# Performance work log

Measured on AMD Instinct MI355X. Metric: run time of the kernel, lower is better.

Reference implementation:

```python
import jax, jax.numpy as jnp
import numpy as np

B, N1, N2 = 2, 1024, 1024
D_MODEL, N_HEADS = 2048, 16
HEAD_DIM = D_MODEL // N_HEADS
EPS = 1e-6
ROPE_THETA = 10000.0


def _split_heads(qkv):
    # [b, n, 3*h*d] -> (q, k, v) each [b, h, n, d]
    b, n, _ = qkv.shape
    qkv = qkv.reshape(b, n, 3, N_HEADS, HEAD_DIM)
    qkv = jnp.transpose(qkv, (2, 0, 3, 1, 4))
    return qkv[0], qkv[1], qkv[2]


def _rmsnorm(x, gamma):
    # RMS norm over head dim with learned scale (QKNorm)
    inv = jax.lax.rsqrt(jnp.mean(jnp.square(x), axis=-1, keepdims=True) + EPS)
    return x * inv * gamma


def _rope(x, offset=0):
    # x: [b, h, n, d]; half-split rotary embedding
    n, d = x.shape[-2], x.shape[-1]
    inv_freq = 1.0 / (ROPE_THETA ** (jnp.arange(0, d, 2, dtype=jnp.float32) / d))
    pos = jnp.arange(n, dtype=jnp.float32) + offset
    ang = pos[:, None] * inv_freq  # [n, d/2]
    cos, sin = jnp.cos(ang), jnp.sin(ang)
    x1, x2 = jnp.split(x, 2, axis=-1)
    return jnp.concatenate([x1 * cos - x2 * sin, x1 * sin + x2 * cos], axis=-1)


def _attention(q, k, v):
    # dense path of flex_attention (block_mask=None): softmax(qk^T/sqrt(d)) v
    scale = 1.0 / np.sqrt(HEAD_DIM)
    scores = jnp.einsum('bhqd,bhkd->bhqk', q, k) * scale
    probs = jax.nn.softmax(scores, axis=-1)
    return jnp.einsum('bhqk,bhkd->bhqd', probs, v)


def setup_inputs() -> dict:
    key = jax.random.key(0)
    ks = jax.random.split(key, 8)
    w_std = 0.02
    return {
        'x_1': jax.random.normal(ks[0], (B, N1, D_MODEL), jnp.float32),
        'x_2': jax.random.normal(ks[1], (B, N2, D_MODEL), jnp.float32),
        'w_qkv1': jax.random.normal(ks[2], (D_MODEL, 3 * D_MODEL), jnp.float32) * w_std,
        'b_qkv1': jnp.zeros((3 * D_MODEL,), jnp.float32),
        'w_qkv2': jax.random.normal(ks[3], (D_MODEL, 3 * D_MODEL), jnp.float32) * w_std,
        'b_qkv2': jnp.zeros((3 * D_MODEL,), jnp.float32),
        'qg1': jnp.ones((HEAD_DIM,), jnp.float32),
        'kg1': jnp.ones((HEAD_DIM,), jnp.float32),
        'qg2': jnp.ones((HEAD_DIM,), jnp.float32),
        'kg2': jnp.ones((HEAD_DIM,), jnp.float32),
        'w_out1': jax.random.normal(ks[4], (D_MODEL, D_MODEL), jnp.float32) * w_std,
        'b_out1': jnp.zeros((D_MODEL,), jnp.float32),
        'w_out2': jax.random.normal(ks[5], (D_MODEL, D_MODEL), jnp.float32) * w_std,
        'b_out2': jnp.zeros((D_MODEL,), jnp.float32),
    }


def reference(x_1, x_2, w_qkv1, b_qkv1, w_qkv2, b_qkv2,
              qg1, kg1, qg2, kg2, w_out1, b_out1, w_out2, b_out2):
    n1 = x_1.shape[1]
    qs, ks_, vs = [], [], []
    for x, w, b, qg, kg in ((x_1, w_qkv1, b_qkv1, qg1, kg1),
                            (x_2, w_qkv2, b_qkv2, qg2, kg2)):
        q, k, v = _split_heads(x @ w + b)
        q, k = _rmsnorm(q, qg), _rmsnorm(k, kg)
        qs.append(q); ks_.append(k); vs.append(v)
    q = jnp.concatenate(qs, axis=-2)  # [b, h, n1+n2, d]
    k = jnp.concatenate(ks_, axis=-2)
    v = jnp.concatenate(vs, axis=-2)
    q, k = _rope(q), _rope(k)
    attn = _attention(q, k, v)
    # merge: b h n d -> b n (h d)
    b, h, n, d = attn.shape
    attn = jnp.transpose(attn, (0, 2, 1, 3)).reshape(b, n, h * d)
    out1 = attn[:, :n1] @ w_out1 + b_out1
    out2 = attn[:, n1:] @ w_out2 + b_out2
    return out1, out2
```

## Files before the change

kernel.cpp:

```cpp
#include <hip/hip_runtime.h>

#define DM   2048
#define NH   16
#define HD   128
#define QKVN 6144
#define NTOT 2048

typedef __bf16 bf16x8 __attribute__((ext_vector_type(8)));
typedef float  f32x4  __attribute__((ext_vector_type(4)));
typedef unsigned short ushort_t;

__device__ __forceinline__ unsigned short f2bf(float f) {
  union { float f; unsigned u; } v; v.f = f;
  return (unsigned short)((v.u + 0x7FFFu + ((v.u >> 16) & 1u)) >> 16);
}
__device__ __forceinline__ float bf2f(unsigned short u) {
  union { unsigned u; float f; } v; v.u = ((unsigned)u) << 16;
  return v.f;
}
__device__ __forceinline__ void glds16(const void* g, void* l) {
  __builtin_amdgcn_global_load_lds(
      (const __attribute__((address_space(1))) unsigned int*)g,
      (__attribute__((address_space(3))) unsigned int*)l, 16, 0, 0);
}
#define COMPILER_MEM_BARRIER() asm volatile("" ::: "memory")


__global__ __launch_bounds__(256) void prep_kernel(
    const float* __restrict__ wq1, const float* __restrict__ wq2,
    const float* __restrict__ wo1, const float* __restrict__ wo2,
    const float* __restrict__ x1,  const float* __restrict__ x2,
    ushort_t* __restrict__ wq1t, ushort_t* __restrict__ wq2t,
    ushort_t* __restrict__ wo1t, ushort_t* __restrict__ wo2t,
    ushort_t* __restrict__ xb1,  ushort_t* __restrict__ xb2,
    float2* __restrict__ rtab)
{
  __shared__ __align__(16) unsigned short Ls[64][72];
  const int bid = blockIdx.x, tid = threadIdx.x;
  if (bid < 8192) {
    const float* src; ushort_t* dst; int N, nb, kb;
    if (bid < 6144) {
      src = (bid < 3072) ? wq1 : wq2; dst = (bid < 3072) ? wq1t : wq2t;
      int id = bid % 3072; N = QKVN; nb = id % 96; kb = id / 96;
    } else {
      int id = bid - 6144;
      src = (id < 1024) ? wo1 : wo2; dst = (id < 1024) ? wo1t : wo2t;
      id %= 1024; N = DM; nb = id % 32; kb = id / 32;
    }
    int n0 = nb * 64, k0 = kb * 64;
#pragma unroll
    for (int it = 0; it < 4; ++it) {
      int row = (tid >> 4) + it * 16, c4 = (tid & 15) * 4;
      float4 v = *reinterpret_cast<const float4*>(&src[(size_t)(k0 + row) * N + n0 + c4]);
      Ls[c4 + 0][row] = f2bf(v.x); Ls[c4 + 1][row] = f2bf(v.y);
      Ls[c4 + 2][row] = f2bf(v.z); Ls[c4 + 3][row] = f2bf(v.w);
    }
    __syncthreads();
#pragma unroll
    for (int it = 0; it < 2; ++it) {
      int lin = tid + it * 256, r = lin >> 3, c8 = (lin & 7) * 8;
      *reinterpret_cast<uint4*>(&dst[(size_t)(n0 + r) * 2048 + k0 + c8]) =
          *reinterpret_cast<const uint4*>(&Ls[r][c8]);
    }
  } else if (bid < 10240) {
    int id = bid - 8192;
    const float* src = (id < 1024) ? x1 : x2;
    ushort_t* dst = (id < 1024) ? xb1 : xb2;
    id %= 1024;
    size_t base = (size_t)id * 4096;
#pragma unroll
    for (int it = 0; it < 4; ++it) {
      size_t i = base + (size_t)(it * 256 + tid) * 4;
      float4 v = *reinterpret_cast<const float4*>(&src[i]);
      ushort4 t; t.x = f2bf(v.x); t.y = f2bf(v.y); t.z = f2bf(v.z); t.w = f2bf(v.w);
      *reinterpret_cast<ushort4*>(&dst[i]) = t;
    }
  } else {
    int id = bid - 10240;
    int e0 = id * 16384;
    for (int i = tid; i < 16384; i += 256) {
      int e = e0 + i; int pos = e >> 6, j = e & 63;
      float ang = (float)pos * exp2f(-(float)j * 0.2076205059304601f);
      float s, c; sincosf(ang, &s, &c);
      rtab[e] = make_float2(c, s);
    }
  }
}

__global__ __launch_bounds__(256) void gemm_qkv_f(
    const ushort_t* __restrict__ Xb, const ushort_t* __restrict__ Wt,
    const float* __restrict__ bias, const float* __restrict__ qg,
    const float* __restrict__ kg, const float2* __restrict__ rtab,
    ushort_t* __restrict__ Q, ushort_t* __restrict__ K,
    ushort_t* __restrict__ VT, int stream_off)
{
  __shared__ __align__(16) union {
    struct { unsigned short a[8192]; unsigned short b[8192]; } s;
    unsigned short c[128][130];
  } L;
  __shared__ float ssq2[128][2];
  const int tid = threadIdx.x, lane = tid & 63, w = tid >> 6;
  const int quad = lane >> 4, l15 = lane & 15;
  const int wrow = (w >> 1) * 64, wcol = (w & 1) * 64;
  const int m0 = blockIdx.y * 128, n0 = blockIdx.x * 128;
  const int lsw = l15 & 7;

  f32x4 acc[4][4];
#pragma unroll
  for (int i = 0; i < 4; i++)
#pragma unroll
    for (int j = 0; j < 4; j++) acc[i][j] = (f32x4){0.f, 0.f, 0.f, 0.f};

  for (int k0 = 0; k0 < DM; k0 += 64) {
#pragma unroll
    for (int it = 0; it < 4; ++it) {
      int c = it * 256 + tid, row = c >> 3, q = (c & 7) ^ (row & 7);
      glds16(&Xb[(size_t)(m0 + row) * 2048 + k0 + q * 8], &L.s.a[c * 8]);
    }
#pragma unroll
    for (int it = 0; it < 4; ++it) {
      int c = it * 256 + tid, row = c >> 3, q = (c & 7) ^ (row & 7);
      glds16(&Wt[(size_t)(n0 + row) * 2048 + k0 + q * 8], &L.s.b[c * 8]);
    }
    __syncthreads();
#pragma unroll
    for (int h = 0; h < 2; ++h) {
      int sq = ((h * 4 + quad) ^ lsw) * 8;
      bf16x8 af[4], bfr[4];
#pragma unroll
      for (int mt = 0; mt < 4; mt++)
        af[mt] = *reinterpret_cast<const bf16x8*>(&L.s.a[(wrow + mt * 16 + l15) * 64 + sq]);
#pragma unroll
      for (int nt = 0; nt < 4; nt++)
        bfr[nt] = *reinterpret_cast<const bf16x8*>(&L.s.b[(wcol + nt * 16 + l15) * 64 + sq]);
#pragma unroll
      for (int mt = 0; mt < 4; mt++)
#pragma unroll
        for (int nt = 0; nt < 4; nt++)
          acc[mt][nt] = __builtin_amdgcn_mfma_f32_16x16x32_bf16(af[mt], bfr[nt], acc[mt][nt], 0, 0, 0);
    }
    __syncthreads();
  }

#pragma unroll
  for (int mt = 0; mt < 4; mt++)
#pragma unroll
    for (int nt = 0; nt < 4; nt++) {
      int col = wcol + nt * 16 + l15;
      float bv = bias[n0 + col];
#pragma unroll
      for (int i = 0; i < 4; i++)
        L.c[wrow + mt * 16 + quad * 4 + i][col] = f2bf(acc[mt][nt][i] + bv);
    }
  __syncthreads();

  const int cc = n0 >> 7, t = cc >> 4, h = cc & 15;
  const int r = tid & 127, half = tid >> 7;
  const int gr = m0 + r, b = gr >> 10;
  const int pos = stream_off + (gr & 1023);
  const int bh = b * NH + h;

  if (t == 2) {
    size_t vb = (size_t)bh * HD * NTOT + pos;
    for (int j = half * 64; j < half * 64 + 64; ++j)
      VT[vb + (size_t)j * NTOT] = L.c[r][j];
  } else {
    float ssq = 0.f;
    for (int j = half * 64; j < half * 64 + 64; ++j) {
      float f = bf2f(L.c[r][j]); ssq += f * f;
    }
    ssq2[r][half] = ssq;
    __syncthreads();
    float inv = rsqrtf((ssq2[r][0] + ssq2[r][1]) * (1.0f / HD) + 1e-6f);
    const float* g = (t == 0) ? qg : kg;
#pragma unroll 4
    for (int jj = 0; jj < 32; ++jj) {
      int j = half * 32 + jj;
      float xv1 = bf2f(L.c[r][j])      * inv * g[j];
      float xv2 = bf2f(L.c[r][j + 64]) * inv * g[j + 64];
      float2 cs = rtab[pos * 64 + j];
      L.c[r][j]      = f2bf(xv1 * cs.x - xv2 * cs.y);
      L.c[r][j + 64] = f2bf(xv1 * cs.y + xv2 * cs.x);
    }
    __syncthreads();
    ushort_t* dst = (t == 0) ? Q : K;
    size_t qb = ((size_t)bh * NTOT + (stream_off + (m0 & 1023))) * HD;
    COMPILER_MEM_BARRIER();
#pragma unroll
    for (int it = 0; it < 32; ++it) {
      int c = it * 256 + tid, rr = c >> 6, cl = c & 63;
      *reinterpret_cast<unsigned int*>(&dst[qb + (size_t)rr * HD + cl * 2]) =
          *reinterpret_cast<const unsigned int*>(&L.c[rr][cl * 2]);
    }
  }
}

__global__ __launch_bounds__(256) void attn_f(
    const ushort_t* __restrict__ Q, const ushort_t* __restrict__ K,
    const ushort_t* __restrict__ VT, ushort_t* __restrict__ O)
{
  __shared__ __align__(16) unsigned short Ks[64 * 128];
  __shared__ __align__(16) unsigned short Vs[128 * 64];
  __shared__ __align__(16) unsigned short Ps[128 * 64];

  const int tid = threadIdx.x, lane = tid & 63, w = tid >> 6;
  const int quad = lane >> 4, l15 = lane & 15;
  const int lsw = l15 & 7;
  const int b = blockIdx.z, h = blockIdx.y;
  const int q0 = blockIdx.x * 128;
  const size_t base = (size_t)(b * NH + h) * NTOT * HD;
  const float scale = 0.088388347648318447f;
  const float SHIFT = 16.0f;

  bf16x8 qf[2][4];
#pragma unroll
  for (int mt = 0; mt < 2; mt++)
#pragma unroll
    for (int ks = 0; ks < 4; ks++)
      qf[mt][ks] = *reinterpret_cast<const bf16x8*>(
          &Q[base + (size_t)(q0 + w * 32 + mt * 16 + l15) * HD + ks * 32 + quad * 8]);

  f32x4 oacc[2][8];
#pragma unroll
  for (int mt = 0; mt < 2; mt++)
#pragma unroll
    for (int nt = 0; nt < 8; nt++) oacc[mt][nt] = (f32x4){0.f, 0.f, 0.f, 0.f};
  float lsum[2][4];
#pragma unroll
  for (int mt = 0; mt < 2; mt++)
#pragma unroll
    for (int i = 0; i < 4; i++) lsum[mt][i] = 0.f;

  for (int kt = 0; kt < NTOT / 64; ++kt) {
#pragma unroll
    for (int it = 0; it < 4; ++it) {
      int c = it * 256 + tid, key = c >> 4, q = (c & 15) ^ (key & 15);
      glds16(&K[base + (size_t)(kt * 64 + key) * HD + q * 8], &Ks[c * 8]);
    }
#pragma unroll
    for (int it = 0; it < 4; ++it) {
      int c = it * 256 + tid, d = c >> 3, q = (c & 7) ^ (d & 7);
      glds16(&VT[base + (size_t)d * NTOT + kt * 64 + q * 8], &Vs[c * 8]);
    }
    __syncthreads();

    f32x4 sacc[2][4];
#pragma unroll
    for (int mt = 0; mt < 2; mt++)
#pragma unroll
      for (int nt = 0; nt < 4; nt++) sacc[mt][nt] = (f32x4){0.f, 0.f, 0.f, 0.f};
#pragma unroll
    for (int ks = 0; ks < 4; ks++) {
      bf16x8 kf[4];
#pragma unroll
      for (int nt = 0; nt < 4; nt++)
        kf[nt] = *reinterpret_cast<const bf16x8*>(
            &Ks[(nt * 16 + l15) * 128 + ((ks * 4 + quad) ^ l15) * 8]);
#pragma unroll
      for (int mt = 0; mt < 2; mt++)
#pragma unroll
        for (int nt = 0; nt < 4; nt++)
          sacc[mt][nt] = __builtin_amdgcn_mfma_f32_16x16x32_bf16(qf[mt][ks], kf[nt], sacc[mt][nt], 0, 0, 0);
    }

#pragma unroll
    for (int mt = 0; mt < 2; mt++)
#pragma unroll
      for (int i = 0; i < 4; i++) {
        int rowl = w * 32 + mt * 16 + quad * 4 + i;
        int rb = (quad * 4 + i) & 7;
#pragma unroll
        for (int nt = 0; nt < 4; nt++) {
          float p = __expf(fmaf(sacc[mt][nt][i], scale, -SHIFT));
          lsum[mt][i] += p;
          Ps[rowl * 64 + (((nt * 2 + (l15 >> 3)) ^ rb) * 8) + (l15 & 7)] = f2bf(p);
        }
      }
    COMPILER_MEM_BARRIER();

#pragma unroll
    for (int kk = 0; kk < 2; kk++) {
      bf16x8 pf[2];
#pragma unroll
      for (int mt = 0; mt < 2; mt++)
        pf[mt] = *reinterpret_cast<const bf16x8*>(
            &Ps[(w * 32 + mt * 16 + l15) * 64 + (((kk * 4 + quad) ^ lsw) * 8)]);
#pragma unroll
      for (int nt = 0; nt < 8; nt++) {
        bf16x8 vf = *reinterpret_cast<const bf16x8*>(
            &Vs[(nt * 16 + l15) * 64 + (((kk * 4 + quad) ^ lsw) * 8)]);
#pragma unroll
        for (int mt = 0; mt < 2; mt++)
          oacc[mt][nt] = __builtin_amdgcn_mfma_f32_16x16x32_bf16(pf[mt], vf, oacc[mt][nt], 0, 0, 0);
      }
    }
    __syncthreads();
  }

#pragma unroll
  for (int mt = 0; mt < 2; mt++)
#pragma unroll
    for (int i = 0; i < 4; i++) {
      float l = lsum[mt][i];
      l += __shfl_xor(l, 1); l += __shfl_xor(l, 2);
      l += __shfl_xor(l, 4); l += __shfl_xor(l, 8);
      float linv = 1.0f / l;
      int qrow = q0 + w * 32 + mt * 16 + quad * 4 + i;
      size_t ob = ((size_t)b * NTOT + qrow) * DM + h * HD;
#pragma unroll
      for (int nt = 0; nt < 8; nt++)
        O[ob + nt * 16 + l15] = f2bf(oacc[mt][nt][i] * linv);
    }
}

__global__ __launch_bounds__(256) void gemm_out_f(
    const ushort_t* __restrict__ A, const ushort_t* __restrict__ Wt,
    const float* __restrict__ bias, float* __restrict__ Out, int stream_off)
{
  __shared__ __align__(16) unsigned short As[8192];
  __shared__ __align__(16) unsigned short Bs[4096];
  const int tid = threadIdx.x, lane = tid & 63, w = tid >> 6;
  const int quad = lane >> 4, l15 = lane & 15;
  const int wrow = (w & 1) * 64, wcol = (w >> 1) * 32;
  const int m0 = blockIdx.y * 128, n0 = blockIdx.x * 64;
  const int lsw = l15 & 7;

  f32x4 acc[4][2];
#pragma unroll
  for (int i = 0; i < 4; i++)
#pragma unroll
    for (int j = 0; j < 2; j++) acc[i][j] = (f32x4){0.f, 0.f, 0.f, 0.f};

  for (int k0 = 0; k0 < DM; k0 += 64) {
#pragma unroll
    for (int it = 0; it < 4; ++it) {
      int c = it * 256 + tid, row = c >> 3, q = (c & 7) ^ (row & 7);
      int gr = m0 + row;
      size_t arow = (size_t)(gr >> 10) * NTOT + stream_off + (gr & 1023);
      glds16(&A[arow * 2048 + k0 + q * 8], &As[c * 8]);
    }
#pragma unroll
    for (int it = 0; it < 2; ++it) {
      int c = it * 256 + tid, row = c >> 3, q = (c & 7) ^ (row & 7);
      glds16(&Wt[(size_t)(n0 + row) * 2048 + k0 + q * 8], &Bs[c * 8]);
    }
    __syncthreads();
#pragma unroll
    for (int h = 0; h < 2; ++h) {
      int sq = ((h * 4 + quad) ^ lsw) * 8;
      bf16x8 af[4], bfr[2];
#pragma unroll
      for (int mt = 0; mt < 4; mt++)
        af[mt] = *reinterpret_cast<const bf16x8*>(&As[(wrow + mt * 16 + l15) * 64 + sq]);
#pragma unroll
      for (int nt = 0; nt < 2; nt++)
        bfr[nt] = *reinterpret_cast<const bf16x8*>(&Bs[(wcol + nt * 16 + l15) * 64 + sq]);
#pragma unroll
      for (int mt = 0; mt < 4; mt++)
#pragma unroll
        for (int nt = 0; nt < 2; nt++)
          acc[mt][nt] = __builtin_amdgcn_mfma_f32_16x16x32_bf16(af[mt], bfr[nt], acc[mt][nt], 0, 0, 0);
    }
    __syncthreads();
  }

#pragma unroll
  for (int mt = 0; mt < 4; mt++)
#pragma unroll
    for (int nt = 0; nt < 2; nt++) {
      int col = n0 + wcol + nt * 16 + l15;
      float bv = bias[col];
#pragma unroll
      for (int i = 0; i < 4; i++) {
        int row = m0 + wrow + mt * 16 + quad * 4 + i;
        Out[(size_t)row * DM + col] = acc[mt][nt][i] + bv;
      }
    }
}

union QkvLdsFb {
  struct { unsigned short a[128][40]; unsigned short b[128][40]; } s;
  unsigned short c[128][130];
};

__global__ __launch_bounds__(256) void gemm_qkv_fb(
    const float* __restrict__ X, const float* __restrict__ W,
    const float* __restrict__ bias, const float* __restrict__ qg,
    const float* __restrict__ kg,
    unsigned short* __restrict__ Q, unsigned short* __restrict__ K,
    unsigned short* __restrict__ V, int stream_off)
{
  __shared__ __align__(16) QkvLdsFb L;
  const int tid = threadIdx.x, lane = tid & 63, wv = tid >> 6;
  const int wrow = (wv >> 1) * 64, wcol = (wv & 1) * 64;
  const int quad = lane >> 4, l15 = lane & 15;
  const int m0 = blockIdx.y * 128, n0 = blockIdx.x * 128;
  f32x4 acc[4][4];
#pragma unroll
  for (int i = 0; i < 4; i++)
#pragma unroll
    for (int j = 0; j < 4; j++) acc[i][j] = (f32x4){0.f, 0.f, 0.f, 0.f};
  for (int k0 = 0; k0 < DM; k0 += 32) {
#pragma unroll
    for (int it = 0; it < 4; ++it) {
      int lin = tid + it * 256, row = lin >> 3, c4 = (lin & 7) * 4;
      float4 av = *reinterpret_cast<const float4*>(&X[(size_t)(m0 + row) * DM + k0 + c4]);
      ushort4 t4; t4.x = f2bf(av.x); t4.y = f2bf(av.y); t4.z = f2bf(av.z); t4.w = f2bf(av.w);
      *reinterpret_cast<ushort4*>(&L.s.a[row][c4]) = t4;
    }
#pragma unroll
    for (int it = 0; it < 4; ++it) {
      int lin = tid + it * 256, kr = lin >> 5, c4 = (lin & 31) * 4;
      float4 wv4 = *reinterpret_cast<const float4*>(&W[(size_t)(k0 + kr) * QKVN + n0 + c4]);
      L.s.b[c4 + 0][kr] = f2bf(wv4.x); L.s.b[c4 + 1][kr] = f2bf(wv4.y);
      L.s.b[c4 + 2][kr] = f2bf(wv4.z); L.s.b[c4 + 3][kr] = f2bf(wv4.w);
    }
    __syncthreads();
    bf16x8 af[4], bfr[4];
#pragma unroll
    for (int mt = 0; mt < 4; mt++)
      af[mt] = *reinterpret_cast<const bf16x8*>(&L.s.a[wrow + mt * 16 + l15][quad * 8]);
#pragma unroll
    for (int nt = 0; nt < 4; nt++)
      bfr[nt] = *reinterpret_cast<const bf16x8*>(&L.s.b[wcol + nt * 16 + l15][quad * 8]);
#pragma unroll
    for (int mt = 0; mt < 4; mt++)
#pragma unroll
      for (int nt = 0; nt < 4; nt++)
        acc[mt][nt] = __builtin_amdgcn_mfma_f32_16x16x32_bf16(af[mt], bfr[nt], acc[mt][nt], 0, 0, 0);
    __syncthreads();
  }
#pragma unroll
  for (int mt = 0; mt < 4; mt++)
#pragma unroll
    for (int nt = 0; nt < 4; nt++) {
      int col = wcol + nt * 16 + l15;
      float bv = bias[n0 + col];
#pragma unroll
      for (int i = 0; i < 4; i++)
        L.c[wrow + mt * 16 + quad * 4 + i][col] = f2bf(acc[mt][nt][i] + bv);
    }
  __syncthreads();
  if (tid < 128) {
    int r = tid, cc = n0 >> 7, t = cc >> 4, h = cc & 15;
    int gr = m0 + r, b = gr >> 10, n = gr & 1023, pos = stream_off + n;
    size_t base = ((size_t)(b * NH + h) * NTOT + pos) * HD;
    if (t == 2) {
      for (int j = 0; j < HD; j++) V[base + j] = L.c[r][j];
    } else {
      float ssq = 0.f;
      for (int j = 0; j < HD; j++) { float f = bf2f(L.c[r][j]); ssq += f * f; }
      float inv = rsqrtf(ssq * (1.0f / HD) + 1e-6f);
      const float* g = (t == 0) ? qg : kg;
      unsigned short* dst = (t == 0) ? Q : K;
      for (int j = 0; j < 64; j++) {
        float x1 = bf2f(L.c[r][j]) * inv * g[j];
        float x2 = bf2f(L.c[r][j + 64]) * inv * g[j + 64];
        float ang = (float)pos * exp2f(-(float)j * 0.2076205059304601f);
        float s, c; sincosf(ang, &s, &c);
        dst[base + j] = f2bf(x1 * c - x2 * s);
        dst[base + j + 64] = f2bf(x1 * s + x2 * c);
      }
    }
  }
}

__global__ __launch_bounds__(256) void attn_fb(
    const unsigned short* __restrict__ Q, const unsigned short* __restrict__ K,
    const unsigned short* __restrict__ V, unsigned short* __restrict__ O)
{
  __shared__ __align__(16) unsigned short Ks[64][136];
  __shared__ __align__(16) unsigned short Vt[128][72];
  __shared__ __align__(16) unsigned short Ps[128][72];
  const int tid = threadIdx.x, lane = tid & 63, w = tid >> 6;
  const int quad = lane >> 4, l15 = lane & 15;
  const int b = blockIdx.z, h = blockIdx.y, q0 = blockIdx.x * 128;
  const size_t base = (size_t)(b * NH + h) * NTOT * HD;
  const float scale = 0.088388347648318447f;
  bf16x8 qf[2][4];
#pragma unroll
  for (int mt = 0; mt < 2; mt++)
#pragma unroll
    for (int ks = 0; ks < 4; ks++)
      qf[mt][ks] = *reinterpret_cast<const bf16x8*>(
          &Q[base + (size_t)(q0 + w * 32 + mt * 16 + l15) * HD + ks * 32 + quad * 8]);
  f32x4 oacc[2][8];
#pragma unroll
  for (int mt = 0; mt < 2; mt++)
#pragma unroll
    for (int nt = 0; nt < 8; nt++) oacc[mt][nt] = (f32x4){0.f, 0.f, 0.f, 0.f};
  float mst[2][4], lst[2][4];
#pragma unroll
  for (int mt = 0; mt < 2; mt++)
#pragma unroll
    for (int i = 0; i < 4; i++) { mst[mt][i] = -1e30f; lst[mt][i] = 0.f; }
  for (int kt = 0; kt < NTOT / 64; ++kt) {
#pragma unroll
    for (int it = 0; it < 4; ++it) {
      int lin = tid + it * 256, kr = lin >> 4, c8 = (lin & 15) * 8;
      uint4 kv = *reinterpret_cast<const uint4*>(&K[base + (size_t)(kt * 64 + kr) * HD + c8]);
      *reinterpret_cast<uint4*>(&Ks[kr][c8]) = kv;
      uint4 vv = *reinterpret_cast<const uint4*>(&V[base + (size_t)(kt * 64 + kr) * HD + c8]);
      const unsigned short* vs = reinterpret_cast<const unsigned short*>(&vv);
#pragma unroll
      for (int j = 0; j < 8; j++) Vt[c8 + j][kr] = vs[j];
    }
    __syncthreads();
    f32x4 sacc[2][4];
#pragma unroll
    for (int mt = 0; mt < 2; mt++)
#pragma unroll
      for (int nt = 0; nt < 4; nt++) sacc[mt][nt] = (f32x4){0.f, 0.f, 0.f, 0.f};
#pragma unroll
    for (int ks = 0; ks < 4; ks++) {
      bf16x8 kf[4];
#pragma unroll
      for (int nt = 0; nt < 4; nt++)
        kf[nt] = *reinterpret_cast<const bf16x8*>(&Ks[nt * 16 + l15][ks * 32 + quad * 8]);
#pragma unroll
      for (int mt = 0; mt < 2; mt++)
#pragma unroll
        for (int nt = 0; nt < 4; nt++)
          sacc[mt][nt] = __builtin_amdgcn_mfma_f32_16x16x32_bf16(qf[mt][ks], kf[nt], sacc[mt][nt], 0, 0, 0);
    }
#pragma unroll
    for (int mt = 0; mt < 2; mt++)
#pragma unroll
      for (int i = 0; i < 4; i++) {
        float sv[4]; float rmax = -1e30f;
#pragma unroll
        for (int nt = 0; nt < 4; nt++) { sv[nt] = sacc[mt][nt][i] * scale; rmax = fmaxf(rmax, sv[nt]); }
        rmax = fmaxf(rmax, __shfl_xor(rmax, 1)); rmax = fmaxf(rmax, __shfl_xor(rmax, 2));
        rmax = fmaxf(rmax, __shfl_xor(rmax, 4)); rmax = fmaxf(rmax, __shfl_xor(rmax, 8));
        float mnew = fmaxf(mst[mt][i], rmax);
        float alpha = __expf(mst[mt][i] - mnew);
        float rsum = 0.f;
#pragma unroll
        for (int nt = 0; nt < 4; nt++) {
          float p = __expf(sv[nt] - mnew); rsum += p;
          Ps[w * 32 + mt * 16 + quad * 4 + i][nt * 16 + l15] = f2bf(p);
        }
        rsum += __shfl_xor(rsum, 1); rsum += __shfl_xor(rsum, 2);
        rsum += __shfl_xor(rsum, 4); rsum += __shfl_xor(rsum, 8);
        lst[mt][i] = lst[mt][i] * alpha + rsum; mst[mt][i] = mnew;
#pragma unroll
        for (int nt = 0; nt < 8; nt++) oacc[mt][nt][i] *= alpha;
      }
    __syncthreads();
#pragma unroll
    for (int kk = 0; kk < 2; kk++) {
      bf16x8 pf[2];
#pragma unroll
      for (int mt = 0; mt < 2; mt++)
        pf[mt] = *reinterpret_cast<const bf16x8*>(&Ps[w * 32 + mt * 16 + l15][kk * 32 + quad * 8]);
#pragma unroll
      for (int nt = 0; nt < 8; nt++) {
        bf16x8 vf = *reinterpret_cast<const bf16x8*>(&Vt[nt * 16 + l15][kk * 32 + quad * 8]);
#pragma unroll
        for (int mt = 0; mt < 2; mt++)
          oacc[mt][nt] = __builtin_amdgcn_mfma_f32_16x16x32_bf16(pf[mt], vf, oacc[mt][nt], 0, 0, 0);
      }
    }
    __syncthreads();
  }
#pragma unroll
  for (int mt = 0; mt < 2; mt++)
#pragma unroll
    for (int i = 0; i < 4; i++) {
      float linv = 1.0f / lst[mt][i];
      int qrow = q0 + w * 32 + mt * 16 + quad * 4 + i;
      size_t ob = ((size_t)b * NTOT + qrow) * DM + h * HD;
#pragma unroll
      for (int nt = 0; nt < 8; nt++)
        O[ob + nt * 16 + l15] = f2bf(oacc[mt][nt][i] * linv);
    }
}

__global__ __launch_bounds__(256) void gemm_out_fb(
    const unsigned short* __restrict__ A, const float* __restrict__ W,
    const float* __restrict__ bias, float* __restrict__ Out, int stream_off)
{
  __shared__ __align__(16) struct { unsigned short a[128][40]; unsigned short b[128][40]; } L;
  const int tid = threadIdx.x, lane = tid & 63, wv = tid >> 6;
  const int wrow = (wv >> 1) * 64, wcol = (wv & 1) * 64;
  const int quad = lane >> 4, l15 = lane & 15;
  const int m0 = blockIdx.y * 128, n0 = blockIdx.x * 128;
  f32x4 acc[4][4];
#pragma unroll
  for (int i = 0; i < 4; i++)
#pragma unroll
    for (int j = 0; j < 4; j++) acc[i][j] = (f32x4){0.f, 0.f, 0.f, 0.f};
  for (int k0 = 0; k0 < DM; k0 += 32) {
#pragma unroll
    for (int it = 0; it < 2; ++it) {
      int lin = tid + it * 256, row = lin >> 2, c8 = (lin & 3) * 8;
      int gr = m0 + row, bb = gr >> 10, n = gr & 1023;
      uint4 av = *reinterpret_cast<const uint4*>(
          &A[(size_t)(bb * NTOT + stream_off + n) * DM + k0 + c8]);
      *reinterpret_cast<uint4*>(&L.a[row][c8]) = av;
    }
#pragma unroll
    for (int it = 0; it < 4; ++it) {
      int lin = tid + it * 256, kr = lin >> 5, c4 = (lin & 31) * 4;
      float4 wv4 = *reinterpret_cast<const float4*>(&W[(size_t)(k0 + kr) * DM + n0 + c4]);
      L.b[c4 + 0][kr] = f2bf(wv4.x); L.b[c4 + 1][kr] = f2bf(wv4.y);
      L.b[c4 + 2][kr] = f2bf(wv4.z); L.b[c4 + 3][kr] = f2bf(wv4.w);
    }
    __syncthreads();
    bf16x8 af[4], bfr[4];
#pragma unroll
    for (int mt = 0; mt < 4; mt++)
      af[mt] = *reinterpret_cast<const bf16x8*>(&L.a[wrow + mt * 16 + l15][quad * 8]);
#pragma unroll
    for (int nt = 0; nt < 4; nt++)
      bfr[nt] = *reinterpret_cast<const bf16x8*>(&L.b[wcol + nt * 16 + l15][quad * 8]);
#pragma unroll
    for (int mt = 0; mt < 4; mt++)
#pragma unroll
      for (int nt = 0; nt < 4; nt++)
        acc[mt][nt] = __builtin_amdgcn_mfma_f32_16x16x32_bf16(af[mt], bfr[nt], acc[mt][nt], 0, 0, 0);
    __syncthreads();
  }
#pragma unroll
  for (int mt = 0; mt < 4; mt++)
#pragma unroll
    for (int nt = 0; nt < 4; nt++) {
      int col = wcol + nt * 16 + l15;
      float bv = bias[n0 + col];
#pragma unroll
      for (int i = 0; i < 4; i++) {
        int row = wrow + mt * 16 + quad * 4 + i;
        Out[(size_t)(m0 + row) * DM + n0 + col] = acc[mt][nt][i] + bv;
      }
    }
}

extern "C" void kernel_launch(void* const* d_in, const int* in_sizes, int n_in,
                              void* d_out, int out_size, void* d_ws, size_t ws_size,
                              hipStream_t stream) {
  (void)in_sizes; (void)n_in; (void)out_size;
  const float* x1  = (const float*)d_in[0];
  const float* x2  = (const float*)d_in[1];
  const float* wq1 = (const float*)d_in[2];
  const float* bq1 = (const float*)d_in[3];
  const float* wq2 = (const float*)d_in[4];
  const float* bq2 = (const float*)d_in[5];
  const float* qg1 = (const float*)d_in[6];
  const float* kg1 = (const float*)d_in[7];
  const float* qg2 = (const float*)d_in[8];
  const float* kg2 = (const float*)d_in[9];
  const float* wo1 = (const float*)d_in[10];
  const float* bo1 = (const float*)d_in[11];
  const float* wo2 = (const float*)d_in[12];
  const float* bo2 = (const float*)d_in[13];
  float* out = (float*)d_out;

  unsigned char* wsb = (unsigned char*)d_ws;
  size_t o = 0;
  auto take = [&](size_t bytes) -> void* {
    void* p = wsb + o; o = (o + bytes + 255) & ~(size_t)255; return p;
  };
  ushort_t* Xb1  = (ushort_t*)take((size_t)4194304 * 2);
  ushort_t* Xb2  = (ushort_t*)take((size_t)4194304 * 2);
  ushort_t* Wq1t = (ushort_t*)take((size_t)12582912 * 2);
  ushort_t* Wq2t = (ushort_t*)take((size_t)12582912 * 2);
  ushort_t* Wo1t = (ushort_t*)take((size_t)4194304 * 2);
  ushort_t* Wo2t = (ushort_t*)take((size_t)4194304 * 2);
  float2*   rtab = (float2*)take((size_t)131072 * 8);
  ushort_t* Qf   = (ushort_t*)take((size_t)8388608 * 2);
  ushort_t* Kf   = (ushort_t*)take((size_t)8388608 * 2);
  ushort_t* VTf  = (ushort_t*)take((size_t)8388608 * 2);
  ushort_t* ATTf = (ushort_t*)take((size_t)8388608 * 2);
  const size_t need = o;

  dim3 blk(256);
  if (ws_size >= need) {
    hipLaunchKernelGGL(prep_kernel, dim3(10248), blk, 0, stream,
                       wq1, wq2, wo1, wo2, x1, x2,
                       Wq1t, Wq2t, Wo1t, Wo2t, Xb1, Xb2, rtab);
    hipLaunchKernelGGL(gemm_qkv_f, dim3(48, 16), blk, 0, stream,
                       Xb1, Wq1t, bq1, qg1, kg1, rtab, Qf, Kf, VTf, 0);
    hipLaunchKernelGGL(gemm_qkv_f, dim3(48, 16), blk, 0, stream,
                       Xb2, Wq2t, bq2, qg2, kg2, rtab, Qf, Kf, VTf, 1024);
    hipLaunchKernelGGL(attn_f, dim3(16, 16, 2), blk, 0, stream, Qf, Kf, VTf, ATTf);
    hipLaunchKernelGGL(gemm_out_f, dim3(32, 16), blk, 0, stream, ATTf, Wo1t, bo1, out, 0);
    hipLaunchKernelGGL(gemm_out_f, dim3(32, 16), blk, 0, stream,
                       ATTf, Wo2t, bo2, out + (size_t)2 * 1024 * DM, 1024);
  } else {
    const size_t QKV_ELEMS = (size_t)2 * NH * NTOT * HD;
    unsigned short* Q   = (unsigned short*)d_ws;
    unsigned short* K   = Q + QKV_ELEMS;
    unsigned short* V   = K + QKV_ELEMS;
    unsigned short* ATT = V + QKV_ELEMS;
    hipLaunchKernelGGL(gemm_qkv_fb, dim3(48, 16), blk, 0, stream, x1, wq1, bq1, qg1, kg1, Q, K, V, 0);
    hipLaunchKernelGGL(gemm_qkv_fb, dim3(48, 16), blk, 0, stream, x2, wq2, bq2, qg2, kg2, Q, K, V, 1024);
    hipLaunchKernelGGL(attn_fb, dim3(16, 16, 2), blk, 0, stream, Q, K, V, ATT);
    hipLaunchKernelGGL(gemm_out_fb, dim3(16, 16), blk, 0, stream, ATT, wo1, bo1, out, 0);
    hipLaunchKernelGGL(gemm_out_fb, dim3(16, 16), blk, 0, stream,
                       ATT, wo2, bo2, out + (size_t)2 * 1024 * DM, 1024);
  }
}
```

Before: 585.4 us.

## Split attention over keys into two halves and merge per-stream launches

Attention is now split into two halves along the key dimension, doubling the grid. Each half writes unnormalised fp32 partial outputs and row sums, and a new combine kernel adds the halves, normalises and writes bf16. This works because the kernel uses a fixed softmax shift rather than a running max. The two QKV GEMM launches and the two output GEMM launches are each merged into one launch using blockIdx.z, which fills more of the GPU per launch. The cost is extra fp32 partial-output traffic and one more kernel. The partial buffers reuse the already-consumed bf16 input and QKV weight workspace, which is fragile if the workspace layout changes.

```diff
diff --git a/kernel.cpp b/kernel.cpp
--- a/kernel.cpp
+++ b/kernel.cpp
@@ -88,17 +88,28 @@
 }
 
 __global__ __launch_bounds__(256) void gemm_qkv_f(
-    const ushort_t* __restrict__ Xb, const ushort_t* __restrict__ Wt,
-    const float* __restrict__ bias, const float* __restrict__ qg,
-    const float* __restrict__ kg, const float2* __restrict__ rtab,
+    const ushort_t* __restrict__ Xb1, const ushort_t* __restrict__ Xb2,
+    const ushort_t* __restrict__ Wt1, const ushort_t* __restrict__ Wt2,
+    const float* __restrict__ bq1, const float* __restrict__ bq2,
+    const float* __restrict__ qg1, const float* __restrict__ kg1,
+    const float* __restrict__ qg2, const float* __restrict__ kg2,
+    const float2* __restrict__ rtab,
     ushort_t* __restrict__ Q, ushort_t* __restrict__ K,
-    ushort_t* __restrict__ VT, int stream_off)
+    ushort_t* __restrict__ VT)
 {
   __shared__ __align__(16) union {
     struct { unsigned short a[8192]; unsigned short b[8192]; } s;
     unsigned short c[128][130];
   } L;
   __shared__ float ssq2[128][2];
+  const int z = blockIdx.z;
+  const ushort_t* Xb = z ? Xb2 : Xb1;
+  const ushort_t* Wt = z ? Wt2 : Wt1;
+  const float* bias = z ? bq2 : bq1;
+  const float* qg = z ? qg2 : qg1;
+  const float* kg = z ? kg2 : kg1;
+  const int stream_off = z * 1024;
+
   const int tid = threadIdx.x, lane = tid & 63, w = tid >> 6;
   const int quad = lane >> 4, l15 = lane & 15;
   const int wrow = (w >> 1) * 64, wcol = (w & 1) * 64;
@@ -197,7 +208,8 @@
 
 __global__ __launch_bounds__(256) void attn_f(
     const ushort_t* __restrict__ Q, const ushort_t* __restrict__ K,
-    const ushort_t* __restrict__ VT, ushort_t* __restrict__ O)
+    const ushort_t* __restrict__ VT,
+    float* __restrict__ Op, float* __restrict__ Lsum)
 {
   __shared__ __align__(16) unsigned short Ks[64 * 128];
   __shared__ __align__(16) unsigned short Vs[128 * 64];
@@ -206,7 +218,9 @@
   const int tid = threadIdx.x, lane = tid & 63, w = tid >> 6;
   const int quad = lane >> 4, l15 = lane & 15;
   const int lsw = l15 & 7;
-  const int b = blockIdx.z, h = blockIdx.y;
+  const int z = blockIdx.z;
+  const int b = z >> 1, split = z & 1;
+  const int h = blockIdx.y;
   const int q0 = blockIdx.x * 128;
   const size_t base = (size_t)(b * NH + h) * NTOT * HD;
   const float scale = 0.088388347648318447f;
@@ -231,7 +245,8 @@
 #pragma unroll
     for (int i = 0; i < 4; i++) lsum[mt][i] = 0.f;
 
-  for (int kt = 0; kt < NTOT / 64; ++kt) {
+  const int kt0 = split * 16;
+  for (int kt = kt0; kt < kt0 + 16; ++kt) {
 #pragma unroll
     for (int it = 0; it < 4; ++it) {
       int c = it * 256 + tid, key = c >> 4, q = (c & 15) ^ (key & 15);
@@ -297,6 +312,7 @@
     __syncthreads();
   }
 
+  const size_t pb = ((size_t)(split * 2 + b) * NH + h) * NTOT;
 #pragma unroll
   for (int mt = 0; mt < 2; mt++)
 #pragma unroll
@@ -304,21 +320,54 @@
       float l = lsum[mt][i];
       l += __shfl_xor(l, 1); l += __shfl_xor(l, 2);
       l += __shfl_xor(l, 4); l += __shfl_xor(l, 8);
-      float linv = 1.0f / l;
       int qrow = q0 + w * 32 + mt * 16 + quad * 4 + i;
-      size_t ob = ((size_t)b * NTOT + qrow) * DM + h * HD;
+      size_t ob = (pb + qrow) * HD;
 #pragma unroll
       for (int nt = 0; nt < 8; nt++)
-        O[ob + nt * 16 + l15] = f2bf(oacc[mt][nt][i] * linv);
-    }
+        Op[ob + nt * 16 + l15] = oacc[mt][nt][i];
+      if (l15 == 0) Lsum[pb + qrow] = l;
+    }
+}
+
+__global__ __launch_bounds__(256) void attn_combine(
+    const float* __restrict__ Op, const float* __restrict__ Lsum,
+    ushort_t* __restrict__ ATT)
+{
+  const int tid = threadIdx.x, r = tid >> 4, c8 = (tid & 15) * 8;
+  const int row = blockIdx.x * 16 + r;
+  const int q = row & 2047, h = (row >> 11) & 15, b = row >> 15;
+  const size_t SPLIT = (size_t)2 * NH * NTOT;
+  const size_t r0 = ((size_t)b * NH + h) * NTOT + q;
+  const size_t r1 = r0 + SPLIT;
+  float linv = 1.0f / (Lsum[r0] + Lsum[r1]);
+  f32x4 a0 = *reinterpret_cast<const f32x4*>(&Op[r0 * HD + c8]);
+  f32x4 a1 = *reinterpret_cast<const f32x4*>(&Op[r0 * HD + c8 + 4]);
+  f32x4 b0 = *reinterpret_cast<const f32x4*>(&Op[r1 * HD + c8]);
+  f32x4 b1 = *reinterpret_cast<const f32x4*>(&Op[r1 * HD + c8 + 4]);
+  ushort_t o[8];
+#pragma unroll
+  for (int j = 0; j < 4; j++) {
+    o[j]     = f2bf((a0[j] + b0[j]) * linv);
+    o[j + 4] = f2bf((a1[j] + b1[j]) * linv);
+  }
+  *reinterpret_cast<uint4*>(&ATT[((size_t)b * NTOT + q) * DM + h * HD + c8]) =
+      *reinterpret_cast<const uint4*>(o);
 }
 
 __global__ __launch_bounds__(256) void gemm_out_f(
-    const ushort_t* __restrict__ A, const ushort_t* __restrict__ Wt,
-    const float* __restrict__ bias, float* __restrict__ Out, int stream_off)
+    const ushort_t* __restrict__ A,
+    const ushort_t* __restrict__ Wt1, const ushort_t* __restrict__ Wt2,
+    const float* __restrict__ bo1, const float* __restrict__ bo2,
+    float* __restrict__ Out)
 {
   __shared__ __align__(16) unsigned short As[8192];
   __shared__ __align__(16) unsigned short Bs[4096];
+  const int z = blockIdx.z;
+  const ushort_t* Wt = z ? Wt2 : Wt1;
+  const float* bias = z ? bo2 : bo1;
+  const int stream_off = z * 1024;
+  float* OutZ = Out + (size_t)z * 2 * 1024 * DM;
+
   const int tid = threadIdx.x, lane = tid & 63, w = tid >> 6;
   const int quad = lane >> 4, l15 = lane & 15;
   const int wrow = (w & 1) * 64, wcol = (w >> 1) * 32;
@@ -373,7 +422,7 @@
 #pragma unroll
       for (int i = 0; i < 4; i++) {
         int row = m0 + wrow + mt * 16 + quad * 4 + i;
-        Out[(size_t)row * DM + col] = acc[mt][nt][i] + bv;
+        OutZ[(size_t)row * DM + col] = acc[mt][nt][i] + bv;
       }
     }
 }
@@ -672,20 +721,21 @@
   ushort_t* VTf  = (ushort_t*)take((size_t)8388608 * 2);
   ushort_t* ATTf = (ushort_t*)take((size_t)8388608 * 2);
   const size_t need = o;
+  float* Op   = (float*)Xb1;
+  float* Lsum = (float*)rtab;
 
   dim3 blk(256);
   if (ws_size >= need) {
     hipLaunchKernelGGL(prep_kernel, dim3(10248), blk, 0, stream,
                        wq1, wq2, wo1, wo2, x1, x2,
                        Wq1t, Wq2t, Wo1t, Wo2t, Xb1, Xb2, rtab);
-    hipLaunchKernelGGL(gemm_qkv_f, dim3(48, 16), blk, 0, stream,
-                       Xb1, Wq1t, bq1, qg1, kg1, rtab, Qf, Kf, VTf, 0);
-    hipLaunchKernelGGL(gemm_qkv_f, dim3(48, 16), blk, 0, stream,
-                       Xb2, Wq2t, bq2, qg2, kg2, rtab, Qf, Kf, VTf, 1024);
-    hipLaunchKernelGGL(attn_f, dim3(16, 16, 2), blk, 0, stream, Qf, Kf, VTf, ATTf);
-    hipLaunchKernelGGL(gemm_out_f, dim3(32, 16), blk, 0, stream, ATTf, Wo1t, bo1, out, 0);
-    hipLaunchKernelGGL(gemm_out_f, dim3(32, 16), blk, 0, stream,
-                       ATTf, Wo2t, bo2, out + (size_t)2 * 1024 * DM, 1024);
+    hipLaunchKernelGGL(gemm_qkv_f, dim3(48, 16, 2), blk, 0, stream,
+                       Xb1, Xb2, Wq1t, Wq2t, bq1, bq2, qg1, kg1, qg2, kg2,
+                       rtab, Qf, Kf, VTf);
+    hipLaunchKernelGGL(attn_f, dim3(16, 16, 4), blk, 0, stream, Qf, Kf, VTf, Op, Lsum);
+    hipLaunchKernelGGL(attn_combine, dim3(4096), blk, 0, stream, Op, Lsum, ATTf);
+    hipLaunchKernelGGL(gemm_out_f, dim3(32, 16, 2), blk, 0, stream,
+                       ATTf, Wo1t, Wo2t, bo1, bo2, out);
   } else {
     const size_t QKV_ELEMS = (size_t)2 * NH * NTOT * HD;
     unsigned short* Q   = (unsigned short*)d_ws;
```

Result: faster. 502.4 us (-14.2%).
